# Kernel tuning notes

Hardware: AMD Instinct MI355X
Metric: run time of the kernel (lower is better)

The kernel has to match this reference:

```python
import jax, jax.numpy as jnp
import numpy as np

N, F_IN, H, MH = 50000, 128, 128, 256
E = 800000

def _lin_init(key, out_d, in_d, bias=True):
    k1, k2 = jax.random.split(key)
    bound = 1.0 / np.sqrt(in_d)
    W = jax.random.uniform(k1, (out_d, in_d), minval=-bound, maxval=bound, dtype=jnp.float32)
    if bias:
        b = jax.random.uniform(k2, (out_d,), minval=-bound, maxval=bound, dtype=jnp.float32)
        return W, b
    return W, None

def setup_inputs() -> dict:
    key = jax.random.key(0)
    ks = jax.random.split(key, 8)
    x = jax.random.normal(ks[0], (N, F_IN), dtype=jnp.float32)
    edge_index = jax.random.randint(ks[1], (2, E), 0, N, dtype=jnp.int64)
    W1l, b1l = _lin_init(ks[2], H, F_IN, bias=True)   # SAGEConv1 neighbor lin (with bias)
    W1r, _ = _lin_init(ks[3], H, F_IN, bias=False)    # SAGEConv1 root lin (no bias)
    W2l, b2l = _lin_init(ks[4], H, H, bias=True)
    W2r, _ = _lin_init(ks[5], H, H, bias=False)
    Wm1, bm1 = _lin_init(ks[6], MH, 2 * H, bias=True)
    Wm2, bm2 = _lin_init(ks[7], 1, MH, bias=True)
    return {"x": x, "edge_index": edge_index,
            "W1l": W1l, "b1l": b1l, "W1r": W1r,
            "W2l": W2l, "b2l": b2l, "W2r": W2r,
            "Wm1": Wm1, "bm1": bm1, "Wm2": Wm2, "bm2": bm2}

def _sage_conv(x, src, dst, Wl, bl, Wr, num_nodes):
    # mean-aggregate messages x[src] at dst, then lin_l(agg) + lin_r(x)
    agg = jax.ops.segment_sum(x[src], dst, num_segments=num_nodes)
    cnt = jax.ops.segment_sum(jnp.ones((src.shape[0],), x.dtype), dst, num_segments=num_nodes)
    agg = agg / jnp.maximum(cnt, 1.0)[:, None]
    return agg @ Wl.T + bl + x @ Wr.T

def reference(x, edge_index, W1l, b1l, W1r, W2l, b2l, W2r, Wm1, bm1, Wm2, bm2):
    src, dst = edge_index[0], edge_index[1]
    n = x.shape[0]
    h = jax.nn.relu(_sage_conv(x, src, dst, W1l, b1l, W1r, n))
    # dropout is identity in eval mode
    h = jax.nn.relu(_sage_conv(h, src, dst, W2l, b2l, W2r, n))
    ef = jnp.concatenate([h[src], h[dst]], axis=-1)  # [E, 2H]
    out = jax.nn.relu(ef @ Wm1.T + bm1) @ Wm2.T + bm2
    return out.reshape(-1)
```

## Files before the change

kernel.cpp:

```cpp
#include <hip/hip_runtime.h>
#include <hip/hip_bf16.h>

#define NN 50000
#define F 128
#define EE 800000
#define MHD 256

typedef __attribute__((ext_vector_type(8))) short bf16x8;
typedef __attribute__((ext_vector_type(4))) float f32x4;

__device__ __forceinline__ float b2f(unsigned short u) {
    union { unsigned int i; float f; } v; v.i = ((unsigned)u) << 16; return v.f;
}
__device__ __forceinline__ unsigned short f2b(float f) {
    unsigned int x = __float_as_uint(f);
    unsigned int r = x + 0x7fffu + ((x >> 16) & 1u);
    return (unsigned short)(r >> 16);
}

__global__ __launch_bounds__(256) void cast_x_kernel(
    const float* __restrict__ in, unsigned short* __restrict__ out) {
    int i = (blockIdx.x * 256 + threadIdx.x) * 4;
    float4 v = *(const float4*)(in + i);
    ushort4 o; o.x = f2b(v.x); o.y = f2b(v.y); o.z = f2b(v.z); o.w = f2b(v.w);
    *(ushort4*)(out + i) = o;
}

__global__ __launch_bounds__(256) void cast_w_kernel(
    const float* __restrict__ W1l, const float* __restrict__ W1r,
    const float* __restrict__ W2l, const float* __restrict__ W2r,
    const float* __restrict__ Wm1, unsigned short* __restrict__ wb) {
    int i = (blockIdx.x * 256 + threadIdx.x) * 4;
    const float* p;
    if (i < 16384)      p = W1l + i;
    else if (i < 32768) p = W1r + (i - 16384);
    else if (i < 49152) p = W2l + (i - 32768);
    else if (i < 65536) p = W2r + (i - 49152);
    else                p = Wm1 + (i - 65536);
    float4 v = *(const float4*)p;
    ushort4 o; o.x = f2b(v.x); o.y = f2b(v.y); o.z = f2b(v.z); o.w = f2b(v.w);
    *(ushort4*)(wb + i) = o;
}

__global__ __launch_bounds__(256) void edge_cvt_hist_kernel(
    const int* __restrict__ ei, int* __restrict__ s32, int* __restrict__ d32,
    int* __restrict__ deg) {
    __shared__ int isI64;
    if (threadIdx.x == 0) {
        int z = 0;
        for (int i = 1; i < 128; i += 2) z |= ei[i];
        isI64 = (z == 0) ? 1 : 0;
    }
    __syncthreads();
    int e = blockIdx.x * 256 + threadIdx.x;
    if (e >= EE) return;
    int s, d;
    if (isI64) {
        const long long* e64 = (const long long*)ei;
        s = (int)e64[e];
        d = (int)e64[EE + e];
    } else {
        s = ei[e];
        d = ei[EE + e];
    }
    s32[e] = s;
    d32[e] = d;
    atomicAdd(&deg[d], 1);
}

__global__ __launch_bounds__(1024) void scan_p1_kernel(
    const int* __restrict__ deg, int* __restrict__ exloc, int* __restrict__ bsum) {
    __shared__ int part[1024];
    int t = threadIdx.x, gid = blockIdx.x * 1024 + t;
    int v = (gid < NN) ? deg[gid] : 0;
    part[t] = v;
    __syncthreads();
    for (int off = 1; off < 1024; off <<= 1) {
        int u = (t >= off) ? part[t - off] : 0;
        __syncthreads();
        part[t] += u;
        __syncthreads();
    }
    exloc[gid] = part[t] - v;
    if (t == 1023) bsum[blockIdx.x] = part[t];
}

__global__ __launch_bounds__(64) void scan_p2_kernel(int* __restrict__ bsum) {
    int t = threadIdx.x;
    int v = (t < 50) ? bsum[t] : 0;
    int orig = v;
    for (int off = 1; off < 64; off <<= 1) {
        int u = __shfl_up(v, off);
        if (t >= off) v += u;
    }
    if (t < 50) bsum[t] = v - orig;
}

__global__ __launch_bounds__(1024) void scan_p3_kernel(
    const int* __restrict__ exloc, const int* __restrict__ bsum,
    int* __restrict__ rowstart, int* __restrict__ cursor) {
    int t = threadIdx.x, gid = blockIdx.x * 1024 + t;
    if (gid > NN) return;
    if (gid == NN) { rowstart[NN] = EE; return; }
    int r = exloc[gid] + bsum[blockIdx.x];
    rowstart[gid] = r;
    cursor[gid] = r;
}

__global__ __launch_bounds__(256) void fill_kernel(
    const int* __restrict__ s32, const int* __restrict__ d32,
    int* __restrict__ cursor, int* __restrict__ nbr, int* __restrict__ eid) {
    int e = blockIdx.x * 256 + threadIdx.x;
    if (e < EE) {
        int p = atomicAdd(&cursor[d32[e]], 1);
        nbr[p] = s32[e];
        eid[p] = e;
    }
}

__global__ __launch_bounds__(256) void agg_gather_kernel(
    const unsigned short* __restrict__ xin,
    const int* __restrict__ nbr, const int* __restrict__ rowstart,
    unsigned short* __restrict__ aggb) {
    int wave = threadIdx.x >> 6, lane = threadIdx.x & 63;
    int node = blockIdx.x * 4 + wave;
    if (node >= NN) return;
    int part = lane >> 4;
    int col8 = (lane & 15) * 8;
    int beg = rowstart[node], end = rowstart[node + 1];
    float a[8] = {0,0,0,0,0,0,0,0};
    float b[8] = {0,0,0,0,0,0,0,0};
    int j = beg + part;
    for (; j + 12 < end; j += 16) {
        int s0 = nbr[j], s1 = nbr[j + 4], s2 = nbr[j + 8], s3 = nbr[j + 12];
        bf16x8 v0 = *(const bf16x8*)(xin + (size_t)s0 * F + col8);
        bf16x8 v1 = *(const bf16x8*)(xin + (size_t)s1 * F + col8);
        bf16x8 v2 = *(const bf16x8*)(xin + (size_t)s2 * F + col8);
        bf16x8 v3 = *(const bf16x8*)(xin + (size_t)s3 * F + col8);
        for (int i = 0; i < 8; i++) a[i] += b2f((unsigned short)v0[i]);
        for (int i = 0; i < 8; i++) b[i] += b2f((unsigned short)v1[i]);
        for (int i = 0; i < 8; i++) a[i] += b2f((unsigned short)v2[i]);
        for (int i = 0; i < 8; i++) b[i] += b2f((unsigned short)v3[i]);
    }
    for (; j < end; j += 4) {
        int s0 = nbr[j];
        bf16x8 v0 = *(const bf16x8*)(xin + (size_t)s0 * F + col8);
        for (int i = 0; i < 8; i++) a[i] += b2f((unsigned short)v0[i]);
    }
    float inv = 1.0f / fmaxf((float)(end - beg), 1.0f);
    unsigned short o[8];
    for (int i = 0; i < 8; i++) {
        float v = a[i] + b[i];
        v += __shfl_xor(v, 16);
        v += __shfl_xor(v, 32);
        o[i] = f2b(v * inv);
    }
    if (part == 0)
        *(bf16x8*)(aggb + (size_t)node * F + col8) = *(bf16x8*)o;
}

__global__ __launch_bounds__(256) void node_gemm_kernel(
    const unsigned short* __restrict__ A1, const unsigned short* __restrict__ A2,
    const unsigned short* __restrict__ W1, const unsigned short* __restrict__ W2,
    const float* __restrict__ bias,
    unsigned short* __restrict__ out) {
    int wave = threadIdx.x >> 6, lane = threadIdx.x & 63;
    int c = lane & 15, q = lane >> 4;
    int m0 = (blockIdx.x * 4 + wave) * 16;
    if (m0 >= NN) return;
    f32x4 acc[8];
    for (int nt = 0; nt < 8; nt++) {
        float b = bias[nt * 16 + c];
        acc[nt] = (f32x4){b, b, b, b};
    }
    int mrow = m0 + c; if (mrow > NN - 1) mrow = NN - 1;
    for (int op = 0; op < 2; op++) {
        const unsigned short* ap = (op ? A2 : A1) + (size_t)mrow * F + q * 8;
        const unsigned short* W  = op ? W2 : W1;
        for (int kb = 0; kb < 4; kb++) {
            bf16x8 a = *(const bf16x8*)(ap + kb * 32);
            for (int nt = 0; nt < 8; nt++) {
                bf16x8 b = *(const bf16x8*)(W + (size_t)(nt * 16 + c) * F + kb * 32 + q * 8);
                acc[nt] = __builtin_amdgcn_mfma_f32_16x16x32_bf16(a, b, acc[nt], 0, 0, 0);
            }
        }
    }
    for (int nt = 0; nt < 8; nt++) {
        for (int r = 0; r < 4; r++) {
            int node = m0 + q * 4 + r;
            if (node < NN) {
                float v = fmaxf(acc[nt][r], 0.0f);
                out[(size_t)node * F + nt * 16 + c] = f2b(v);
            }
        }
    }
}

__global__ __launch_bounds__(256) void pq_gemm_kernel(
    const unsigned short* __restrict__ h,
    const unsigned short* __restrict__ wmb,
    const float* __restrict__ bm1,
    unsigned short* __restrict__ PQ) {
    int wave = threadIdx.x >> 6, lane = threadIdx.x & 63;
    int c = lane & 15, q = lane >> 4;
    int half = wave >> 1, ntBase = (wave & 1) * 8;
    int m0 = blockIdx.x * 16;
    int mrow = m0 + c; if (mrow > NN - 1) mrow = NN - 1;
    bf16x8 a[4];
#pragma unroll
    for (int kb = 0; kb < 4; kb++)
        a[kb] = *(const bf16x8*)(h + (size_t)mrow * F + kb * 32 + q * 8);
    f32x4 acc[8];
#pragma unroll
    for (int nt = 0; nt < 8; nt++) {
        float b = half ? bm1[(ntBase + nt) * 16 + c] : 0.0f;
        acc[nt] = (f32x4){b, b, b, b};
    }
#pragma unroll
    for (int kb = 0; kb < 4; kb++) {
#pragma unroll
        for (int nt = 0; nt < 8; nt++) {
            bf16x8 b = *(const bf16x8*)(wmb + (size_t)((ntBase + nt) * 16 + c) * 256 + half * 128 + kb * 32 + q * 8);
            acc[nt] = __builtin_amdgcn_mfma_f32_16x16x32_bf16(a[kb], b, acc[nt], 0, 0, 0);
        }
    }
#pragma unroll
    for (int r = 0; r < 4; r++) {
        int node = m0 + q * 4 + r;
        if (node < NN) {
            unsigned short o[8];
#pragma unroll
            for (int nt = 0; nt < 8; nt++) o[nt] = f2b(acc[nt][r]);
            *(bf16x8*)(PQ + (size_t)node * 512 + half * 256 + c * 16 + ntBase) = *(bf16x8*)o;
        }
    }
}

__global__ __launch_bounds__(256) void edge_dot_kernel(
    const unsigned short* __restrict__ PQ,
    const int* __restrict__ nbr, const int* __restrict__ eid,
    const int* __restrict__ rowstart,
    const float* __restrict__ Wm2, const float* __restrict__ bm2,
    float* __restrict__ out) {
    int wave = threadIdx.x >> 6, lane = threadIdx.x & 63;
    int node = blockIdx.x * 4 + wave;
    if (node >= NN) return;
    int g = lane >> 4, l16 = lane & 15;
    int col = l16 * 16;
    float w2f[16], qf[16];
#pragma unroll
    for (int i = 0; i < 16; i++) w2f[i] = Wm2[i * 16 + l16];
    {
        bf16x8 q0 = *(const bf16x8*)(PQ + (size_t)node * 512 + 256 + col);
        bf16x8 q1 = *(const bf16x8*)(PQ + (size_t)node * 512 + 256 + col + 8);
#pragma unroll
        for (int i = 0; i < 8; i++) { qf[i] = b2f((unsigned short)q0[i]); qf[8 + i] = b2f((unsigned short)q1[i]); }
    }
    float b2 = bm2[0];
    int beg = rowstart[node], end = rowstart[node + 1];
    int j = beg + g;
    for (; j + 4 < end; j += 8) {
        int s0 = nbr[j], s1 = nbr[j + 4];
        int id0 = eid[j], id1 = eid[j + 4];
        uint4 a0 = *(const uint4*)(PQ + (size_t)s0 * 512 + col);
        uint4 a1 = *(const uint4*)(PQ + (size_t)s0 * 512 + col + 8);
        uint4 c0 = *(const uint4*)(PQ + (size_t)s1 * 512 + col);
        uint4 c1 = *(const uint4*)(PQ + (size_t)s1 * 512 + col + 8);
        float t0 = 0.f, t1 = 0.f;
        unsigned int w0[8] = {a0.x, a0.y, a0.z, a0.w, a1.x, a1.y, a1.z, a1.w};
        unsigned int w1[8] = {c0.x, c0.y, c0.z, c0.w, c1.x, c1.y, c1.z, c1.w};
#pragma unroll
        for (int i = 0; i < 8; i++) {
            float lo0 = __uint_as_float(w0[i] << 16);
            float hi0 = __uint_as_float(w0[i] & 0xffff0000u);
            float lo1 = __uint_as_float(w1[i] << 16);
            float hi1 = __uint_as_float(w1[i] & 0xffff0000u);
            t0 += fmaxf(lo0 + qf[2 * i], 0.f) * w2f[2 * i]
                + fmaxf(hi0 + qf[2 * i + 1], 0.f) * w2f[2 * i + 1];
            t1 += fmaxf(lo1 + qf[2 * i], 0.f) * w2f[2 * i]
                + fmaxf(hi1 + qf[2 * i + 1], 0.f) * w2f[2 * i + 1];
        }
        t0 += __shfl_xor(t0, 1);  t1 += __shfl_xor(t1, 1);
        t0 += __shfl_xor(t0, 2);  t1 += __shfl_xor(t1, 2);
        t0 += __shfl_xor(t0, 4);  t1 += __shfl_xor(t1, 4);
        t0 += __shfl_xor(t0, 8);  t1 += __shfl_xor(t1, 8);
        if (l16 == 0) { out[id0] = t0 + b2; out[id1] = t1 + b2; }
    }
    for (; j < end; j += 4) {
        int s = nbr[j];
        int id = eid[j];
        uint4 a0 = *(const uint4*)(PQ + (size_t)s * 512 + col);
        uint4 a1 = *(const uint4*)(PQ + (size_t)s * 512 + col + 8);
        unsigned int w0[8] = {a0.x, a0.y, a0.z, a0.w, a1.x, a1.y, a1.z, a1.w};
        float t = 0.f;
#pragma unroll
        for (int i = 0; i < 8; i++) {
            float lo = __uint_as_float(w0[i] << 16);
            float hi = __uint_as_float(w0[i] & 0xffff0000u);
            t += fmaxf(lo + qf[2 * i], 0.f) * w2f[2 * i]
               + fmaxf(hi + qf[2 * i + 1], 0.f) * w2f[2 * i + 1];
        }
        t += __shfl_xor(t, 1);
        t += __shfl_xor(t, 2);
        t += __shfl_xor(t, 4);
        t += __shfl_xor(t, 8);
        if (l16 == 0) out[id] = t + b2;
    }
}

extern "C" void kernel_launch(void* const* d_in, const int* in_sizes, int n_in,
                              void* d_out, int out_size, void* d_ws, size_t ws_size,
                              hipStream_t stream) {
    const float* x   = (const float*)d_in[0];
    const int*   ei  = (const int*)d_in[1];
    const float* W1l = (const float*)d_in[2];
    const float* b1l = (const float*)d_in[3];
    const float* W1r = (const float*)d_in[4];
    const float* W2l = (const float*)d_in[5];
    const float* b2l = (const float*)d_in[6];
    const float* W2r = (const float*)d_in[7];
    const float* Wm1 = (const float*)d_in[8];
    const float* bm1 = (const float*)d_in[9];
    const float* Wm2 = (const float*)d_in[10];
    const float* bm2 = (const float*)d_in[11];

    char* ws = (char*)d_ws;
    unsigned short* PQ       = (unsigned short*)(ws);
    unsigned short* xb       = (unsigned short*)(ws);
    unsigned short* h1       = (unsigned short*)(ws + 12800000);
    unsigned short* aggb     = (unsigned short*)(ws + 25600000);
    unsigned short* wb       = (unsigned short*)(ws + 51200000);
    int*            s32      = (int*)(ws + 51462144);
    int*            d32      = (int*)(ws + 54662144);
    int*            deg      = (int*)(ws + 57862144);
    int*            rowstart = (int*)(ws + 58062208);
    int*            cursor   = (int*)(ws + 58262272);
    int*            nbr      = (int*)(ws + 58462336);
    int*            eid      = (int*)(ws + 61662336);
    unsigned short* h2       = (unsigned short*)(ws + 64862336);
    int*            exloc    = (int*)(ws + 77662336);
    int*            bsum     = (int*)(ws + 77867136);
    float*          outp     = (float*)d_out;

    const unsigned short* w1l_b = wb;
    const unsigned short* w1r_b = wb + 16384;
    const unsigned short* w2l_b = wb + 32768;
    const unsigned short* w2r_b = wb + 49152;
    const unsigned short* wm1_b = wb + 65536;

    cast_x_kernel<<<6250, 256, 0, stream>>>(x, xb);
    cast_w_kernel<<<128, 256, 0, stream>>>(W1l, W1r, W2l, W2r, Wm1, wb);
    hipMemsetAsync(deg, 0, 200064, stream);
    edge_cvt_hist_kernel<<<3125, 256, 0, stream>>>(ei, s32, d32, deg);
    scan_p1_kernel<<<50, 1024, 0, stream>>>(deg, exloc, bsum);
    scan_p2_kernel<<<1, 64, 0, stream>>>(bsum);
    scan_p3_kernel<<<50, 1024, 0, stream>>>(exloc, bsum, rowstart, cursor);
    fill_kernel<<<3125, 256, 0, stream>>>(s32, d32, cursor, nbr, eid);

    agg_gather_kernel<<<12500, 256, 0, stream>>>(xb, nbr, rowstart, aggb);
    node_gemm_kernel<<<782, 256, 0, stream>>>(aggb, xb, w1l_b, w1r_b, b1l, h1);
    agg_gather_kernel<<<12500, 256, 0, stream>>>(h1, nbr, rowstart, aggb);
    node_gemm_kernel<<<782, 256, 0, stream>>>(aggb, h1, w2l_b, w2r_b, b2l, h2);
    pq_gemm_kernel<<<3125, 256, 0, stream>>>(h2, wm1_b, bm1, PQ);
    edge_dot_kernel<<<12500, 256, 0, stream>>>(PQ, nbr, eid, rowstart, Wm2, bm2, outp);
}
```

Baseline: 443.5 us.

## Permute hidden-feature layout for vector stores, fold scan pass, unroll gather tail

The node GEMM epilogue now writes each row's eight bf16 outputs as one 16-byte vector store instead of scattered 2-byte stores. Hidden features are therefore stored in a permuted column order, and the layer-2 and MLP weight K dimensions are permuted to match at cast time. The single-block scan_p2 kernel is removed; each scan_p3 block sums the preceding block totals serially, saving one launch. The gather tail loop is unrolled by two with dual accumulators. This relies on the permutation being consistent across every consumer of h1 and h2, including the edge-dot kernel.

Result: no change. 436.1 us (-1.7%).

```diff
diff --git a/kernel.cpp b/kernel.cpp
--- a/kernel.cpp
+++ b/kernel.cpp
@@ -31,15 +31,32 @@
     const float* __restrict__ W2l, const float* __restrict__ W2r,
     const float* __restrict__ Wm1, unsigned short* __restrict__ wb) {
     int i = (blockIdx.x * 256 + threadIdx.x) * 4;
-    const float* p;
-    if (i < 16384)      p = W1l + i;
-    else if (i < 32768) p = W1r + (i - 16384);
-    else if (i < 49152) p = W2l + (i - 32768);
-    else if (i < 65536) p = W2r + (i - 49152);
-    else                p = Wm1 + (i - 65536);
-    float4 v = *(const float4*)p;
-    ushort4 o; o.x = f2b(v.x); o.y = f2b(v.y); o.z = f2b(v.z); o.w = f2b(v.w);
-    *(ushort4*)(wb + i) = o;
+    unsigned short o[4];
+    if (i < 32768) {
+        const float* p = (i < 16384) ? (W1l + i) : (W1r + (i - 16384));
+        float4 v = *(const float4*)p;
+        o[0] = f2b(v.x); o[1] = f2b(v.y); o[2] = f2b(v.z); o[3] = f2b(v.w);
+    } else if (i < 65536) {
+        int local = i - 32768;
+        const float* M = (local < 16384) ? W2l : W2r;
+        int lm = local & 16383;
+        int n = lm >> 7, kp = lm & 127;
+#pragma unroll
+        for (int t = 0; t < 4; t++) {
+            int k = ((kp + t) & 7) * 16 + ((kp + t) >> 3);
+            o[t] = f2b(M[n * 128 + k]);
+        }
+    } else {
+        int local = i - 65536;
+        int n = local >> 8, k2 = local & 255;
+        int half = k2 >> 7, kp = k2 & 127;
+#pragma unroll
+        for (int t = 0; t < 4; t++) {
+            int k = half * 128 + ((kp + t) & 7) * 16 + ((kp + t) >> 3);
+            o[t] = f2b(Wm1[n * 256 + k]);
+        }
+    }
+    *(ushort4*)(wb + i) = *(ushort4*)o;
 }
 
 __global__ __launch_bounds__(256) void edge_cvt_hist_kernel(
@@ -85,24 +102,20 @@
     if (t == 1023) bsum[blockIdx.x] = part[t];
 }
 
-__global__ __launch_bounds__(64) void scan_p2_kernel(int* __restrict__ bsum) {
-    int t = threadIdx.x;
-    int v = (t < 50) ? bsum[t] : 0;
-    int orig = v;
-    for (int off = 1; off < 64; off <<= 1) {
-        int u = __shfl_up(v, off);
-        if (t >= off) v += u;
-    }
-    if (t < 50) bsum[t] = v - orig;
-}
-
 __global__ __launch_bounds__(1024) void scan_p3_kernel(
     const int* __restrict__ exloc, const int* __restrict__ bsum,
     int* __restrict__ rowstart, int* __restrict__ cursor) {
-    int t = threadIdx.x, gid = blockIdx.x * 1024 + t;
+    __shared__ int offs;
+    if (threadIdx.x == 0) {
+        int s = 0;
+        for (int b = 0; b < blockIdx.x; b++) s += bsum[b];
+        offs = s;
+    }
+    __syncthreads();
+    int gid = blockIdx.x * 1024 + threadIdx.x;
     if (gid > NN) return;
     if (gid == NN) { rowstart[NN] = EE; return; }
-    int r = exloc[gid] + bsum[blockIdx.x];
+    int r = exloc[gid] + offs;
     rowstart[gid] = r;
     cursor[gid] = r;
 }
@@ -142,7 +155,14 @@
         for (int i = 0; i < 8; i++) a[i] += b2f((unsigned short)v2[i]);
         for (int i = 0; i < 8; i++) b[i] += b2f((unsigned short)v3[i]);
     }
-    for (; j < end; j += 4) {
+    for (; j + 4 < end; j += 8) {
+        int s0 = nbr[j], s1 = nbr[j + 4];
+        bf16x8 v0 = *(const bf16x8*)(xin + (size_t)s0 * F + col8);
+        bf16x8 v1 = *(const bf16x8*)(xin + (size_t)s1 * F + col8);
+        for (int i = 0; i < 8; i++) a[i] += b2f((unsigned short)v0[i]);
+        for (int i = 0; i < 8; i++) b[i] += b2f((unsigned short)v1[i]);
+    }
+    if (j < end) {
         int s0 = nbr[j];
         bf16x8 v0 = *(const bf16x8*)(xin + (size_t)s0 * F + col8);
         for (int i = 0; i < 8; i++) a[i] += b2f((unsigned short)v0[i]);
@@ -185,13 +205,14 @@
             }
         }
     }
-    for (int nt = 0; nt < 8; nt++) {
-        for (int r = 0; r < 4; r++) {
-            int node = m0 + q * 4 + r;
-            if (node < NN) {
-                float v = fmaxf(acc[nt][r], 0.0f);
-                out[(size_t)node * F + nt * 16 + c] = f2b(v);
-            }
+#pragma unroll
+    for (int r = 0; r < 4; r++) {
+        int node = m0 + q * 4 + r;
+        if (node < NN) {
+            unsigned short o[8];
+#pragma unroll
+            for (int nt = 0; nt < 8; nt++) o[nt] = f2b(fmaxf(acc[nt][r], 0.0f));
+            *(bf16x8*)(out + (size_t)node * F + c * 8) = *(bf16x8*)o;
         }
     }
 }
@@ -342,25 +363,24 @@
     int*            bsum     = (int*)(ws + 77867136);
     float*          outp     = (float*)d_out;
 
-    const unsigned short* w1l_b = wb;
-    const unsigned short* w1r_b = wb + 16384;
-    const unsigned short* w2l_b = wb + 32768;
-    const unsigned short* w2r_b = wb + 49152;
-    const unsigned short* wm1_b = wb + 65536;
+    const unsigned short* w1l_b  = wb;
+    const unsigned short* w1r_b  = wb + 16384;
+    const unsigned short* w2l_p  = wb + 32768;
+    const unsigned short* w2r_p  = wb + 49152;
+    const unsigned short* wm1_p  = wb + 65536;
 
     cast_x_kernel<<<6250, 256, 0, stream>>>(x, xb);
     cast_w_kernel<<<128, 256, 0, stream>>>(W1l, W1r, W2l, W2r, Wm1, wb);
     hipMemsetAsync(deg, 0, 200064, stream);
     edge_cvt_hist_kernel<<<3125, 256, 0, stream>>>(ei, s32, d32, deg);
     scan_p1_kernel<<<50, 1024, 0, stream>>>(deg, exloc, bsum);
-    scan_p2_kernel<<<1, 64, 0, stream>>>(bsum);
     scan_p3_kernel<<<50, 1024, 0, stream>>>(exloc, bsum, rowstart, cursor);
     fill_kernel<<<3125, 256, 0, stream>>>(s32, d32, cursor, nbr, eid);
 
     agg_gather_kernel<<<12500, 256, 0, stream>>>(xb, nbr, rowstart, aggb);
     node_gemm_kernel<<<782, 256, 0, stream>>>(aggb, xb, w1l_b, w1r_b, b1l, h1);
     agg_gather_kernel<<<12500, 256, 0, stream>>>(h1, nbr, rowstart, aggb);
-    node_gemm_kernel<<<782, 256, 0, stream>>>(aggb, h1, w2l_b, w2r_b, b2l, h2);
-    pq_gemm_kernel<<<3125, 256, 0, stream>>>(h2, wm1_b, bm1, PQ);
+    node_gemm_kernel<<<782, 256, 0, stream>>>(aggb, h1, w2l_p, w2r_p, b2l, h2);
+    pq_gemm_kernel<<<3125, 256, 0, stream>>>(h2, wm1_p, bm1, PQ);
     edge_dot_kernel<<<12500, 256, 0, stream>>>(PQ, nbr, eid, rowstart, Wm2, bm2, outp);
 }
```
